# Optimization experiments

Measured on AMD Instinct MI355X. Metric: run time of the kernel, lower is better.

The kernel has to match this reference:

```python
import jax, jax.numpy as jnp
import numpy as np

SPATIAL_SHAPES = [(58, 100)]  # single level (H, W)
N_HEADS, N_LEVELS, N_POINTS, NUM_CAMS = 8, 1, 8, 6
D_MODEL = 256


def _bilinear_sample(v, loc, h, w):
    # v: (B, h, w, H, d); loc: (B, Lq, H, P, 2) normalized to [0,1]
    # matches F.grid_sample(mode='bilinear', padding_mode='zeros', align_corners=False)
    x = loc[..., 0] * w - 0.5
    y = loc[..., 1] * h - 0.5
    x0 = jnp.floor(x)
    y0 = jnp.floor(y)
    fx = x - x0
    fy = y - y0
    x0i = x0.astype(jnp.int32)
    y0i = y0.astype(jnp.int32)
    B, Hh = v.shape[0], v.shape[3]
    b = jnp.arange(B)[:, None, None, None]
    hd = jnp.arange(Hh)[None, None, :, None]

    def g(yi, xi):
        valid = ((yi >= 0) & (yi < h) & (xi >= 0) & (xi < w)).astype(v.dtype)
        yc = jnp.clip(yi, 0, h - 1)
        xc = jnp.clip(xi, 0, w - 1)
        return v[b, yc, xc, hd] * valid[..., None]  # (B,Lq,H,P,d)

    return (g(y0i, x0i) * ((1 - fy) * (1 - fx))[..., None]
            + g(y0i, x0i + 1) * ((1 - fy) * fx)[..., None]
            + g(y0i + 1, x0i) * (fy * (1 - fx))[..., None]
            + g(y0i + 1, x0i + 1) * (fy * fx)[..., None])


def _ms_deform_attn(value, locs, weights):
    # value: (B, S, H, d); locs: (B,Lq,H,L,P,2); weights: (B,Lq,H,L,P)
    B, S, Hh, d = value.shape
    out = 0.0
    start = 0
    for l, (h, w) in enumerate(SPATIAL_SHAPES):
        v = value[:, start:start + h * w].reshape(B, h, w, Hh, d)
        start += h * w
        samp = _bilinear_sample(v, locs[:, :, :, l], h, w)  # (B,Lq,H,P,d)
        out = out + jnp.einsum('bqhpd,bqhp->bqhd', samp, weights[:, :, :, l])
    return out.reshape(B, -1, Hh * d)


def setup_inputs() -> dict:
    key = jax.random.key(0)
    ks = jax.random.split(key, 12)
    B, Lq, C = 1, 22500, D_MODEL
    S = sum(h * w for h, w in SPATIAL_SHAPES)
    inp = {
        'query': jax.random.normal(ks[0], (B, Lq, C), jnp.float32),
        'reference_points_cam': jax.random.uniform(ks[1], (NUM_CAMS, B, Lq, 4, 2), jnp.float32),
        'bev_mask': jax.random.randint(ks[2], (NUM_CAMS, B, Lq, 4), 0, 2, jnp.int32),
        'value': jax.random.normal(ks[3], (B * NUM_CAMS, S, C), jnp.float32),
        'W_off': jax.random.normal(ks[4], (N_HEADS * N_LEVELS * N_POINTS * 2, C), jnp.float32) * 0.01,
        'b_off': jax.random.normal(ks[5], (N_HEADS * N_LEVELS * N_POINTS * 2,), jnp.float32),
        'W_attn': jax.random.normal(ks[6], (N_HEADS * N_LEVELS * N_POINTS, C), jnp.float32) * 0.02,
        'b_attn': jnp.zeros((N_HEADS * N_LEVELS * N_POINTS,), jnp.float32),
        'W_val': jax.random.normal(ks[7], (C, C), jnp.float32) * (1.0 / np.sqrt(C)),
        'b_val': jnp.zeros((C,), jnp.float32),
        'W_out': jax.random.normal(ks[8], (C, C), jnp.float32) * (1.0 / np.sqrt(C)),
        'b_out': jnp.zeros((C,), jnp.float32),
    }
    return inp


def reference(query, reference_points_cam, bev_mask, value,
              W_off, b_off, W_attn, b_attn, W_val, b_val, W_out, b_out):
    B, Lq, C = query.shape
    d = C // N_HEADS
    D = reference_points_cam.shape[3]  # num_Z_anchors = 4
    S = value.shape[1]

    # value_proj for all cameras; value rows are laid out as b*num_cams + cam
    val = value @ W_val.T + b_val
    val = val.reshape(B, NUM_CAMS, S, N_HEADS, d).transpose(1, 0, 2, 3, 4)  # (cams,B,S,H,d)

    # query-side projections are camera-independent
    off = (query @ W_off.T + b_off).reshape(B, Lq, N_HEADS, N_LEVELS, N_POINTS, 2)
    normalizer = jnp.array([[w, h] for (h, w) in SPATIAL_SHAPES], dtype=query.dtype)  # (L,2)
    off = off / normalizer[None, None, None, :, None, :]
    off = off.reshape(B, Lq, N_HEADS, N_LEVELS, N_POINTS // D, D, 2)

    aw = (query @ W_attn.T + b_attn).reshape(B, Lq, N_HEADS, N_LEVELS * N_POINTS)
    aw = jax.nn.softmax(aw, axis=-1).reshape(B, Lq, N_HEADS, N_LEVELS, N_POINTS)

    vis = (bev_mask.sum(-1) > 0)  # (cams, B, Lq)
    slots = jnp.zeros_like(query)
    for cam in range(NUM_CAMS):  # small fixed camera set
        ref = reference_points_cam[cam][:, :, None, None, None, :, :]  # (B,Lq,1,1,1,D,2)
        locs = (ref + off).reshape(B, Lq, N_HEADS, N_LEVELS, N_POINTS, 2)
        out = _ms_deform_attn(val[cam], locs, aw)  # (B,Lq,C)
        slots = slots + out * vis[cam][..., None].astype(query.dtype)

    count = jnp.maximum(vis.sum(0).astype(query.dtype), 1.0)  # (B,Lq)
    slots = slots / count[..., None]
    return slots @ W_out.T + b_out
```

## Files before the change

kernel.cpp:

```cpp
#include <hip/hip_runtime.h>

#define LQ     22500
#define SPA_H  58
#define SPA_W  100
#define S_TOT  5800
#define NCAMS  6
#define CDIM   256

typedef __attribute__((ext_vector_type(8))) _Float16 half8;
typedef __attribute__((ext_vector_type(4))) float f32x4;

__device__ __forceinline__ half8 cvt_f32x8(const float* p) {
  f32x4 a = *(const f32x4*)p;
  f32x4 b = *(const f32x4*)(p + 4);
  half8 r;
  r[0] = (_Float16)a.x; r[1] = (_Float16)a.y; r[2] = (_Float16)a.z; r[3] = (_Float16)a.w;
  r[4] = (_Float16)b.x; r[5] = (_Float16)b.y; r[6] = (_Float16)b.z; r[7] = (_Float16)b.w;
  return r;
}

__global__ __launch_bounds__(256) void cvt_weights_all(
    const float* __restrict__ Wv, const float* __restrict__ Wo,
    const float* __restrict__ Wf, const float* __restrict__ Wa,
    const float* __restrict__ bf, const float* __restrict__ ba,
    _Float16* __restrict__ dst, float* __restrict__ biascat) {
  const int i = blockIdx.x * 256 + threadIdx.x;
  if (i < 192) biascat[i] = (i < 128) ? bf[i] : ba[i - 128];
  if (i >= 180224) return;
  float v;
  if (i < 65536)       v = Wv[i];
  else if (i < 131072) v = Wo[i - 65536];
  else { const int j = i - 131072; v = (j < 32768) ? Wf[j] : Wa[j - 32768]; }
  dst[i] = (_Float16)v;
}

template<int N, bool A_F16, int OUT_MODE>
__global__ __launch_bounds__(256, 2) void gemm64(
    const void* __restrict__ Av, const _Float16* __restrict__ W,
    const float* __restrict__ bias, void* __restrict__ Cv, int M) {
  constexpr int K  = CDIM;
  constexpr int NT = (N / 4) / 16;
  const int lane = threadIdx.x & 63;
  const int wave = threadIdx.x >> 6;
  const int m15  = lane & 15;
  const int quad = lane >> 4;
  const int rowbase = blockIdx.x * 64;
  const int colbase = wave * (N / 4);

  f32x4 acc[4][NT];
#pragma unroll
  for (int rt = 0; rt < 4; ++rt)
#pragma unroll
    for (int t = 0; t < NT; ++t) acc[rt][t] = (f32x4){0.f, 0.f, 0.f, 0.f};

#pragma unroll
  for (int kk = 0; kk < K; kk += 32) {
    const int ko = kk + quad * 8;
    half8 a[4], b[NT];
#pragma unroll
    for (int rt = 0; rt < 4; ++rt) {
      int row = rowbase + rt * 16 + m15;
      row = row < M ? row : M - 1;
      if (A_F16) a[rt] = *(const half8*)((const _Float16*)Av + (size_t)row * K + ko);
      else       a[rt] = cvt_f32x8((const float*)Av + (size_t)row * K + ko);
    }
#pragma unroll
    for (int t = 0; t < NT; ++t)
      b[t] = *(const half8*)(W + (size_t)(colbase + t * 16 + m15) * K + ko);
#pragma unroll
    for (int t = 0; t < NT; ++t)
#pragma unroll
      for (int rt = 0; rt < 4; ++rt)
        acc[rt][t] = __builtin_amdgcn_mfma_f32_16x16x32_f16(a[rt], b[t], acc[rt][t], 0, 0, 0);
  }

#pragma unroll
  for (int rt = 0; rt < 4; ++rt) {
    const int orow = rowbase + rt * 16 + quad * 4;
#pragma unroll
    for (int t = 0; t < NT; ++t) {
      const int col = colbase + t * 16 + m15;
      const float bv = bias[col];
#pragma unroll
      for (int i = 0; i < 4; ++i) {
        const int r = orow + i;
        if (r < M) {
          const float v = acc[rt][t][i] + bv;
          if (OUT_MODE == 0) ((float*)Cv)[(size_t)r * N + col] = v;
          else               ((_Float16*)Cv)[(size_t)r * N + col] = (_Float16)v;
        }
      }
    }
  }
}

__global__ __launch_bounds__(128) void sampler(
    const _Float16* __restrict__ vp,
    const _Float16* __restrict__ qproj,
    const float* __restrict__ ref,
    const int* __restrict__ bev,
    _Float16* __restrict__ slots)
{
  const int t  = threadIdx.x;
  const int ql = t >> 4;
  const int s  = t & 15;
  const int h  = s >> 1;
  const int hf = s & 1;
  const int q  = blockIdx.x * 8 + ql;
  const bool qok = q < LQ;

  __shared__ float s_off[8][128];
  __shared__ float s_aw[8][64];
  __shared__ float s_ref[8][48];
  __shared__ int   s_vis[8][6];

  if (s < 6) s_vis[ql][s] = 0;
  if (qok) {
    const _Float16* qp = qproj + (size_t)q * 192;
#pragma unroll
    for (int rep = 0; rep < 12; ++rep) {
      const int j = s + rep * 16;
      const float v = (float)qp[j];
      if (j < 128) s_off[ql][j] = v * ((j & 1) ? (1.f / 58.f) : (1.f / 100.f));
      else         s_aw[ql][j - 128] = v;
    }
#pragma unroll
    for (int rep = 0; rep < 3; ++rep) {
      const int k = s + rep * 16;
      s_ref[ql][k] = ref[((size_t)(k >> 3) * LQ + q) * 8 + (k & 7)];
    }
    if (s < 6) {
      const int* bm = bev + ((size_t)s * LQ + q) * 4;
      s_vis[ql][s] = (bm[0] + bm[1] + bm[2] + bm[3]) > 0 ? 1 : 0;
    }
  }
  __syncthreads();

  float w8[8];
  {
    float m = -1e30f;
#pragma unroll
    for (int p = 0; p < 8; ++p) m = fmaxf(m, s_aw[ql][h * 8 + p]);
    float ssum = 0.f;
#pragma unroll
    for (int p = 0; p < 8; ++p) { w8[p] = __expf(s_aw[ql][h * 8 + p] - m); ssum += w8[p]; }
    const float inv = 1.f / ssum;
#pragma unroll
    for (int p = 0; p < 8; ++p) w8[p] *= inv;
  }

  int cnt = 0;
#pragma unroll
  for (int c = 0; c < 6; ++c) cnt += s_vis[ql][c];
  const float invc = 1.f / (float)(cnt > 0 ? cnt : 1);

  float acc[16];
#pragma unroll
  for (int i = 0; i < 16; ++i) acc[i] = 0.f;

  const int chbase = h * 32 + hf * 16;

#pragma unroll
  for (int cam = 0; cam < NCAMS; ++cam) {
    if (!s_vis[ql][cam]) continue;
    const _Float16* vpc = vp + (size_t)cam * (S_TOT * CDIM) + chbase;
#pragma unroll
    for (int p = 0; p < 8; ++p) {
      const int z = p & 3;
      const float lx = s_ref[ql][cam * 8 + z * 2 + 0] + s_off[ql][(h * 8 + p) * 2 + 0];
      const float ly = s_ref[ql][cam * 8 + z * 2 + 1] + s_off[ql][(h * 8 + p) * 2 + 1];
      const float x = lx * 100.f - 0.5f;
      const float y = ly * 58.f - 0.5f;
      const float x0f = floorf(x), y0f = floorf(y);
      const float fx = x - x0f, fy = y - y0f;
      const int x0 = (int)x0f, y0 = (int)y0f;
      const float wgt = w8[p];
      const float w00 = (1.f - fy) * (1.f - fx) * wgt;
      const float w01 = (1.f - fy) * fx * wgt;
      const float w10 = fy * (1.f - fx) * wgt;
      const float w11 = fy * fx * wgt;
      const bool xv0 = (x0 >= 0) && (x0 < SPA_W);
      const bool xv1 = (x0 + 1 >= 0) && (x0 + 1 < SPA_W);
#pragma unroll
      for (int dy = 0; dy < 2; ++dy) {
        const int yy = y0 + dy;
        if (yy < 0 || yy >= SPA_H) continue;
        const _Float16* rowp = vpc + (size_t)(yy * SPA_W) * CDIM;
        const float wl = dy ? w10 : w00;
        const float wr = dy ? w11 : w01;
        if (xv0) {
          const _Float16* tp = rowp + (size_t)x0 * CDIM;
          half8 v0 = *(const half8*)tp;
          half8 v1 = *(const half8*)(tp + 8);
#pragma unroll
          for (int i = 0; i < 8; ++i) acc[i]     = fmaf(wl, (float)v0[i], acc[i]);
#pragma unroll
          for (int i = 0; i < 8; ++i) acc[8 + i] = fmaf(wl, (float)v1[i], acc[8 + i]);
        }
        if (xv1) {
          const _Float16* tp = rowp + (size_t)(x0 + 1) * CDIM;
          half8 v0 = *(const half8*)tp;
          half8 v1 = *(const half8*)(tp + 8);
#pragma unroll
          for (int i = 0; i < 8; ++i) acc[i]     = fmaf(wr, (float)v0[i], acc[i]);
#pragma unroll
          for (int i = 0; i < 8; ++i) acc[8 + i] = fmaf(wr, (float)v1[i], acc[8 + i]);
        }
      }
    }
  }

  if (qok) {
    half8 o0, o1;
#pragma unroll
    for (int i = 0; i < 8; ++i) { o0[i] = (_Float16)(acc[i] * invc); o1[i] = (_Float16)(acc[8 + i] * invc); }
    _Float16* sp = slots + (size_t)q * CDIM + chbase;
    *(half8*)sp = o0;
    *(half8*)(sp + 8) = o1;
  }
}

extern "C" void kernel_launch(void* const* d_in, const int* in_sizes, int n_in,
                              void* d_out, int out_size, void* d_ws, size_t ws_size,
                              hipStream_t stream) {
  const float* query  = (const float*)d_in[0];
  const float* refpts = (const float*)d_in[1];
  const int*   bev    = (const int*)d_in[2];
  const float* value  = (const float*)d_in[3];
  const float* W_off  = (const float*)d_in[4];
  const float* b_off  = (const float*)d_in[5];
  const float* W_attn = (const float*)d_in[6];
  const float* b_attn = (const float*)d_in[7];
  const float* W_val  = (const float*)d_in[8];
  const float* b_val  = (const float*)d_in[9];
  const float* W_out  = (const float*)d_in[10];
  const float* b_out  = (const float*)d_in[11];

  char* ws = (char*)d_ws;
  _Float16* Wv_h    = (_Float16*)(ws + 0);
  _Float16* Wo_h    = (_Float16*)(ws + 131072);
  _Float16* Wcat_h  = (_Float16*)(ws + 262144);
  float*    biascat = (float*)   (ws + 360448);
  _Float16* vp      = (_Float16*)(ws + 361216);
  _Float16* qproj   = (_Float16*)(ws + 18178816);
  _Float16* slots   = (_Float16*)(ws + 26818816);

  cvt_weights_all<<<704, 256, 0, stream>>>(W_val, W_out, W_off, W_attn,
                                           b_off, b_attn, Wv_h, biascat);

  gemm64<256, false, 2><<<(34800 + 63) / 64, 256, 0, stream>>>(value, Wv_h, b_val, vp, 34800);
  gemm64<192, false, 2><<<(LQ + 63) / 64, 256, 0, stream>>>(query, Wcat_h, biascat, qproj, LQ);

  sampler<<<(LQ + 7) / 8, 128, 0, stream>>>(vp, qproj, refpts, bev, slots);

  gemm64<256, true, 0><<<(LQ + 63) / 64, 256, 0, stream>>>(slots, Wo_h, b_out, d_out, LQ);
}
```

Measured before the change: 370.9 us.

## Pre-convert inputs to fp16, fuse input GEMMs, pipeline K loop, branchless sampler

Converts value and query to fp16 in one vectorized pass, then runs the value and query projections in a single fused launch that writes results in place over the fp16 inputs, using a block barrier before the stores. The GEMM K loop is double-buffered with explicit load/MFMA interleaving. The sampler precomputes the softmax once per head in shared memory, uses clamped branchless bilinear taps with four loads issued together, and reuses the query buffer for slots. This reduces launches, workspace and f32 read traffic in the GEMMs and improves memory-level parallelism in the sampler, at the cost of an extra full conversion pass and aliasing risks.

```diff
diff --git a/kernel.cpp b/kernel.cpp
--- a/kernel.cpp
+++ b/kernel.cpp
@@ -8,44 +8,55 @@
 #define CDIM   256
 
 typedef __attribute__((ext_vector_type(8))) _Float16 half8;
+typedef __attribute__((ext_vector_type(4))) _Float16 half4;
 typedef __attribute__((ext_vector_type(4))) float f32x4;
 
-__device__ __forceinline__ half8 cvt_f32x8(const float* p) {
-  f32x4 a = *(const f32x4*)p;
-  f32x4 b = *(const f32x4*)(p + 4);
-  half8 r;
-  r[0] = (_Float16)a.x; r[1] = (_Float16)a.y; r[2] = (_Float16)a.z; r[3] = (_Float16)a.w;
-  r[4] = (_Float16)b.x; r[5] = (_Float16)b.y; r[6] = (_Float16)b.z; r[7] = (_Float16)b.w;
-  return r;
-}
-
-__global__ __launch_bounds__(256) void cvt_weights_all(
-    const float* __restrict__ Wv, const float* __restrict__ Wo,
-    const float* __restrict__ Wf, const float* __restrict__ Wa,
-    const float* __restrict__ bf, const float* __restrict__ ba,
-    _Float16* __restrict__ dst, float* __restrict__ biascat) {
-  const int i = blockIdx.x * 256 + threadIdx.x;
-  if (i < 192) biascat[i] = (i < 128) ? bf[i] : ba[i - 128];
-  if (i >= 180224) return;
-  float v;
-  if (i < 65536)       v = Wv[i];
-  else if (i < 131072) v = Wo[i - 65536];
-  else { const int j = i - 131072; v = (j < 32768) ? Wf[j] : Wa[j - 32768]; }
-  dst[i] = (_Float16)v;
-}
-
-template<int N, bool A_F16, int OUT_MODE>
-__global__ __launch_bounds__(256, 2) void gemm64(
-    const void* __restrict__ Av, const _Float16* __restrict__ W,
-    const float* __restrict__ bias, void* __restrict__ Cv, int M) {
-  constexpr int K  = CDIM;
-  constexpr int NT = (N / 4) / 16;
+__global__ __launch_bounds__(256) void cvt_all(
+    const float* __restrict__ value, const float* __restrict__ query,
+    const float* __restrict__ W_val, const float* __restrict__ W_off,
+    const float* __restrict__ W_attn, const float* __restrict__ W_out,
+    _Float16* __restrict__ val16, _Float16* __restrict__ q16,
+    _Float16* __restrict__ Wv, _Float16* __restrict__ Wcat,
+    _Float16* __restrict__ Wo) {
+  const long long e = ((long long)blockIdx.x * 256 + threadIdx.x) * 4;
+  const float* src; _Float16* dst; long long off;
+  if (e < 8908800)        { src = value;  dst = val16;        off = e; }
+  else if (e < 14668800)  { src = query;  dst = q16;          off = e - 8908800; }
+  else if (e < 14734336)  { src = W_val;  dst = Wv;           off = e - 14668800; }
+  else if (e < 14767104)  { src = W_off;  dst = Wcat;         off = e - 14734336; }
+  else if (e < 14783488)  { src = W_attn; dst = Wcat + 32768; off = e - 14767104; }
+  else if (e < 14849024)  { src = W_out;  dst = Wo;           off = e - 14783488; }
+  else return;
+  f32x4 v = *(const f32x4*)(src + off);
+  half4 o;
+  o[0] = (_Float16)v.x; o[1] = (_Float16)v.y; o[2] = (_Float16)v.z; o[3] = (_Float16)v.w;
+  *(half4*)(dst + off) = o;
+}
+
+template<int N, int OUT_MODE, bool INPLACE>
+__device__ __forceinline__ void gemm_body(
+    const _Float16* __restrict__ A, const _Float16* __restrict__ W,
+    const float* __restrict__ bias, const float* __restrict__ bias2,
+    void* __restrict__ Cv, int M, int rowbase) {
+  constexpr int NT = N / 64;
   const int lane = threadIdx.x & 63;
   const int wave = threadIdx.x >> 6;
   const int m15  = lane & 15;
   const int quad = lane >> 4;
-  const int rowbase = blockIdx.x * 64;
   const int colbase = wave * (N / 4);
+  const int kq = quad * 8;
+
+  const _Float16* ap[4];
+#pragma unroll
+  for (int rt = 0; rt < 4; ++rt) {
+    int r = rowbase + rt * 16 + m15;
+    r = r < M ? r : M - 1;
+    ap[rt] = A + (size_t)r * 256 + kq;
+  }
+  const _Float16* wp[NT];
+#pragma unroll
+  for (int t = 0; t < NT; ++t)
+    wp[t] = W + (size_t)(colbase + t * 16 + m15) * 256 + kq;
 
   f32x4 acc[4][NT];
 #pragma unroll
@@ -53,26 +64,30 @@
 #pragma unroll
     for (int t = 0; t < NT; ++t) acc[rt][t] = (f32x4){0.f, 0.f, 0.f, 0.f};
 
-#pragma unroll
-  for (int kk = 0; kk < K; kk += 32) {
-    const int ko = kk + quad * 8;
-    half8 a[4], b[NT];
-#pragma unroll
-    for (int rt = 0; rt < 4; ++rt) {
-      int row = rowbase + rt * 16 + m15;
-      row = row < M ? row : M - 1;
-      if (A_F16) a[rt] = *(const half8*)((const _Float16*)Av + (size_t)row * K + ko);
-      else       a[rt] = cvt_f32x8((const float*)Av + (size_t)row * K + ko);
-    }
-#pragma unroll
-    for (int t = 0; t < NT; ++t)
-      b[t] = *(const half8*)(W + (size_t)(colbase + t * 16 + m15) * K + ko);
-#pragma unroll
-    for (int t = 0; t < NT; ++t)
-#pragma unroll
-      for (int rt = 0; rt < 4; ++rt)
-        acc[rt][t] = __builtin_amdgcn_mfma_f32_16x16x32_f16(a[rt], b[t], acc[rt][t], 0, 0, 0);
-  }
+  half8 a0[4], b0[NT], a1[4], b1[NT];
+#define LOADSET(aa, bb, KO) \
+  { _Pragma("unroll") for (int rt = 0; rt < 4; ++rt) aa[rt] = *(const half8*)(ap[rt] + (KO)); \
+    _Pragma("unroll") for (int t = 0; t < NT; ++t)  bb[t]  = *(const half8*)(wp[t] + (KO)); }
+#define MFMASET(aa, bb) \
+  { _Pragma("unroll") for (int t = 0; t < NT; ++t) \
+      _Pragma("unroll") for (int rt = 0; rt < 4; ++rt) \
+        acc[rt][t] = __builtin_amdgcn_mfma_f32_16x16x32_f16(aa[rt], bb[t], acc[rt][t], 0, 0, 0); }
+
+  LOADSET(a0, b0, 0)
+#pragma unroll 1
+  for (int kk = 0; kk < 192; kk += 64) {
+    LOADSET(a1, b1, kk + 32)
+    MFMASET(a0, b0)
+    LOADSET(a0, b0, kk + 64)
+    MFMASET(a1, b1)
+  }
+  LOADSET(a1, b1, 224)
+  MFMASET(a0, b0)
+  MFMASET(a1, b1)
+#undef LOADSET
+#undef MFMASET
+
+  if (INPLACE) __syncthreads();
 
 #pragma unroll
   for (int rt = 0; rt < 4; ++rt) {
@@ -80,18 +95,35 @@
 #pragma unroll
     for (int t = 0; t < NT; ++t) {
       const int col = colbase + t * 16 + m15;
-      const float bv = bias[col];
+      const float bv = (N == 192 && col >= 128) ? bias2[col - 128] : bias[col];
 #pragma unroll
       for (int i = 0; i < 4; ++i) {
         const int r = orow + i;
         if (r < M) {
           const float v = acc[rt][t][i] + bv;
-          if (OUT_MODE == 0) ((float*)Cv)[(size_t)r * N + col] = v;
-          else               ((_Float16*)Cv)[(size_t)r * N + col] = (_Float16)v;
+          if (OUT_MODE == 0) ((float*)Cv)[(size_t)r * 256 + col] = v;
+          else               ((_Float16*)Cv)[(size_t)r * 256 + col] = (_Float16)v;
         }
       }
     }
   }
+}
+
+__global__ __launch_bounds__(256) void gemm_inputs(
+    const _Float16* __restrict__ val16, const _Float16* __restrict__ q16,
+    const _Float16* __restrict__ Wv, const _Float16* __restrict__ Wcat,
+    const float* __restrict__ b_val, const float* __restrict__ b_off,
+    const float* __restrict__ b_attn,
+    _Float16* __restrict__ vp, _Float16* __restrict__ qproj) {
+  const int b = blockIdx.x;
+  if (b < 544) gemm_body<256, 2, true>(val16, Wv, b_val, b_val, vp, 34800, b * 64);
+  else         gemm_body<192, 2, true>(q16, Wcat, b_off, b_attn, qproj, LQ, (b - 544) * 64);
+}
+
+__global__ __launch_bounds__(256) void gemm_out_k(
+    const _Float16* __restrict__ slots, const _Float16* __restrict__ Wo,
+    const float* __restrict__ b_out, float* __restrict__ out) {
+  gemm_body<256, 0, false>(slots, Wo, b_out, b_out, out, LQ, blockIdx.x * 64);
 }
 
 __global__ __launch_bounds__(128) void sampler(
@@ -105,49 +137,49 @@
   const int ql = t >> 4;
   const int s  = t & 15;
   const int h  = s >> 1;
-  const int hf = s & 1;
   const int q  = blockIdx.x * 8 + ql;
   const bool qok = q < LQ;
 
-  __shared__ float s_off[8][128];
-  __shared__ float s_aw[8][64];
+  __shared__ float s_off[8][8][17];
+  __shared__ float s_w8[8][8][9];
   __shared__ float s_ref[8][48];
   __shared__ int   s_vis[8][6];
 
-  if (s < 6) s_vis[ql][s] = 0;
   if (qok) {
-    const _Float16* qp = qproj + (size_t)q * 192;
-#pragma unroll
-    for (int rep = 0; rep < 12; ++rep) {
-      const int j = s + rep * 16;
-      const float v = (float)qp[j];
-      if (j < 128) s_off[ql][j] = v * ((j & 1) ? (1.f / 58.f) : (1.f / 100.f));
-      else         s_aw[ql][j - 128] = v;
-    }
-#pragma unroll
-    for (int rep = 0; rep < 3; ++rep) {
-      const int k = s + rep * 16;
-      s_ref[ql][k] = ref[((size_t)(k >> 3) * LQ + q) * 8 + (k & 7)];
+    const _Float16* qp = qproj + (size_t)q * 256;
+    {
+      half8 oc = *(const half8*)(qp + s * 8);
+#pragma unroll
+      for (int i = 0; i < 8; ++i) {
+        const int f = s * 8 + i;
+        s_off[ql][f >> 4][f & 15] =
+            (float)oc[i] * ((f & 1) ? (1.f / 58.f) : (1.f / 100.f));
+      }
+    }
+    if (s < 8) {
+      half8 aw = *(const half8*)(qp + 128 + s * 8);
+      float m = -1e30f;
+#pragma unroll
+      for (int p = 0; p < 8; ++p) m = fmaxf(m, (float)aw[p]);
+      float e[8], ssum = 0.f;
+#pragma unroll
+      for (int p = 0; p < 8; ++p) { e[p] = __expf((float)aw[p] - m); ssum += e[p]; }
+      const float inv = 1.f / ssum;
+#pragma unroll
+      for (int p = 0; p < 8; ++p) s_w8[ql][s][p] = e[p] * inv;
+    }
+    if (s < 12) {
+      const int cam = s >> 1, hf = s & 1;
+      f32x4 r = *(const f32x4*)(ref + ((size_t)cam * LQ + q) * 8 + hf * 4);
+      *(f32x4*)&s_ref[ql][s * 4] = r;
     }
     if (s < 6) {
-      const int* bm = bev + ((size_t)s * LQ + q) * 4;
-      s_vis[ql][s] = (bm[0] + bm[1] + bm[2] + bm[3]) > 0 ? 1 : 0;
+      int4 bm = *(const int4*)(bev + ((size_t)s * LQ + q) * 4);
+      s_vis[ql][s] = (bm.x + bm.y + bm.z + bm.w) > 0 ? 1 : 0;
     }
   }
   __syncthreads();
-
-  float w8[8];
-  {
-    float m = -1e30f;
-#pragma unroll
-    for (int p = 0; p < 8; ++p) m = fmaxf(m, s_aw[ql][h * 8 + p]);
-    float ssum = 0.f;
-#pragma unroll
-    for (int p = 0; p < 8; ++p) { w8[p] = __expf(s_aw[ql][h * 8 + p] - m); ssum += w8[p]; }
-    const float inv = 1.f / ssum;
-#pragma unroll
-    for (int p = 0; p < 8; ++p) w8[p] *= inv;
-  }
+  if (!qok) return;
 
   int cnt = 0;
 #pragma unroll
@@ -158,66 +190,68 @@
 #pragma unroll
   for (int i = 0; i < 16; ++i) acc[i] = 0.f;
 
-  const int chbase = h * 32 + hf * 16;
-
-#pragma unroll
+#pragma unroll 1
   for (int cam = 0; cam < NCAMS; ++cam) {
     if (!s_vis[ql][cam]) continue;
-    const _Float16* vpc = vp + (size_t)cam * (S_TOT * CDIM) + chbase;
-#pragma unroll
-    for (int p = 0; p < 8; ++p) {
-      const int z = p & 3;
-      const float lx = s_ref[ql][cam * 8 + z * 2 + 0] + s_off[ql][(h * 8 + p) * 2 + 0];
-      const float ly = s_ref[ql][cam * 8 + z * 2 + 1] + s_off[ql][(h * 8 + p) * 2 + 1];
-      const float x = lx * 100.f - 0.5f;
-      const float y = ly * 58.f - 0.5f;
-      const float x0f = floorf(x), y0f = floorf(y);
-      const float fx = x - x0f, fy = y - y0f;
-      const int x0 = (int)x0f, y0 = (int)y0f;
-      const float wgt = w8[p];
-      const float w00 = (1.f - fy) * (1.f - fx) * wgt;
-      const float w01 = (1.f - fy) * fx * wgt;
-      const float w10 = fy * (1.f - fx) * wgt;
-      const float w11 = fy * fx * wgt;
-      const bool xv0 = (x0 >= 0) && (x0 < SPA_W);
-      const bool xv1 = (x0 + 1 >= 0) && (x0 + 1 < SPA_W);
-#pragma unroll
-      for (int dy = 0; dy < 2; ++dy) {
-        const int yy = y0 + dy;
-        if (yy < 0 || yy >= SPA_H) continue;
-        const _Float16* rowp = vpc + (size_t)(yy * SPA_W) * CDIM;
-        const float wl = dy ? w10 : w00;
-        const float wr = dy ? w11 : w01;
-        if (xv0) {
-          const _Float16* tp = rowp + (size_t)x0 * CDIM;
-          half8 v0 = *(const half8*)tp;
-          half8 v1 = *(const half8*)(tp + 8);
-#pragma unroll
-          for (int i = 0; i < 8; ++i) acc[i]     = fmaf(wl, (float)v0[i], acc[i]);
-#pragma unroll
-          for (int i = 0; i < 8; ++i) acc[8 + i] = fmaf(wl, (float)v1[i], acc[8 + i]);
+    const _Float16* vpc = vp + (size_t)cam * (S_TOT * CDIM) + s * 16;
+
+#pragma unroll 1
+    for (int pp = 0; pp < 4; ++pp) {
+      half8 v[16];
+      float w[8];
+#pragma unroll
+      for (int j = 0; j < 2; ++j) {
+        const int p = pp * 2 + j;
+        const int z = p & 3;
+        const float x = (s_ref[ql][cam * 8 + z * 2 + 0] + s_off[ql][h][p * 2 + 0]) * 100.f - 0.5f;
+        const float y = (s_ref[ql][cam * 8 + z * 2 + 1] + s_off[ql][h][p * 2 + 1]) * 58.f - 0.5f;
+        const float x0f = floorf(x), y0f = floorf(y);
+        const float fx = x - x0f, fy = y - y0f;
+        const int x0 = (int)x0f, y0 = (int)y0f;
+        const float vx0 = (x0 >= 0 && x0 < SPA_W) ? 1.f : 0.f;
+        const float vx1 = (x0 >= -1 && x0 < SPA_W - 1) ? 1.f : 0.f;
+        const float vy0 = (y0 >= 0 && y0 < SPA_H) ? 1.f : 0.f;
+        const float vy1 = (y0 >= -1 && y0 < SPA_H - 1) ? 1.f : 0.f;
+        const int xc0 = min(max(x0, 0), SPA_W - 1), xc1 = min(max(x0 + 1, 0), SPA_W - 1);
+        const int yc0 = min(max(y0, 0), SPA_H - 1), yc1 = min(max(y0 + 1, 0), SPA_H - 1);
+        const float wgt = s_w8[ql][h][p];
+        const float wy0 = (1.f - fy) * wgt, wy1 = fy * wgt;
+        w[j * 4 + 0] = wy0 * (1.f - fx) * vy0 * vx0;
+        w[j * 4 + 1] = wy0 * fx * vy0 * vx1;
+        w[j * 4 + 2] = wy1 * (1.f - fx) * vy1 * vx0;
+        w[j * 4 + 3] = wy1 * fx * vy1 * vx1;
+        const _Float16* t00 = vpc + (size_t)(yc0 * SPA_W + xc0) * CDIM;
+        const _Float16* t01 = vpc + (size_t)(yc0 * SPA_W + xc1) * CDIM;
+        const _Float16* t10 = vpc + (size_t)(yc1 * SPA_W + xc0) * CDIM;
+        const _Float16* t11 = vpc + (size_t)(yc1 * SPA_W + xc1) * CDIM;
+        v[j * 8 + 0] = *(const half8*)t00; v[j * 8 + 1] = *(const half8*)(t00 + 8);
+        v[j * 8 + 2] = *(const half8*)t01; v[j * 8 + 3] = *(const half8*)(t01 + 8);
+        v[j * 8 + 4] = *(const half8*)t10; v[j * 8 + 5] = *(const half8*)(t10 + 8);
+        v[j * 8 + 6] = *(const half8*)t11; v[j * 8 + 7] = *(const half8*)(t11 + 8);
+      }
+#pragma unroll
+      for (int j = 0; j < 2; ++j)
+#pragma unroll
+        for (int tap = 0; tap < 4; ++tap) {
+          const float wk = w[j * 4 + tap];
+#pragma unroll
+          for (int i = 0; i < 8; ++i) {
+            acc[i]     = fmaf(wk, (float)v[j * 8 + tap * 2][i],     acc[i]);
+            acc[8 + i] = fmaf(wk, (float)v[j * 8 + tap * 2 + 1][i], acc[8 + i]);
+          }
         }
-        if (xv1) {
-          const _Float16* tp = rowp + (size_t)(x0 + 1) * CDIM;
-          half8 v0 = *(const half8*)tp;
-          half8 v1 = *(const half8*)(tp + 8);
-#pragma unroll
-          for (int i = 0; i < 8; ++i) acc[i]     = fmaf(wr, (float)v0[i], acc[i]);
-#pragma unroll
-          for (int i = 0; i < 8; ++i) acc[8 + i] = fmaf(wr, (float)v1[i], acc[8 + i]);
-        }
-      }
-    }
-  }
-
-  if (qok) {
-    half8 o0, o1;
-#pragma unroll
-    for (int i = 0; i < 8; ++i) { o0[i] = (_Float16)(acc[i] * invc); o1[i] = (_Float16)(acc[8 + i] * invc); }
-    _Float16* sp = slots + (size_t)q * CDIM + chbase;
-    *(half8*)sp = o0;
-    *(half8*)(sp + 8) = o1;
-  }
+    }
+  }
+
+  half8 o0, o1;
+#pragma unroll
+  for (int i = 0; i < 8; ++i) {
+    o0[i] = (_Float16)(acc[i] * invc);
+    o1[i] = (_Float16)(acc[8 + i] * invc);
+  }
+  _Float16* sp = slots + (size_t)q * 256 + s * 16;
+  *(half8*)sp = o0;
+  *(half8*)(sp + 8) = o1;
 }
 
 extern "C" void kernel_launch(void* const* d_in, const int* in_sizes, int n_in,
@@ -237,21 +271,19 @@
   const float* b_out  = (const float*)d_in[11];
 
   char* ws = (char*)d_ws;
-  _Float16* Wv_h    = (_Float16*)(ws + 0);
-  _Float16* Wo_h    = (_Float16*)(ws + 131072);
-  _Float16* Wcat_h  = (_Float16*)(ws + 262144);
-  float*    biascat = (float*)   (ws + 360448);
-  _Float16* vp      = (_Float16*)(ws + 361216);
-  _Float16* qproj   = (_Float16*)(ws + 18178816);
-  _Float16* slots   = (_Float16*)(ws + 26818816);
-
-  cvt_weights_all<<<704, 256, 0, stream>>>(W_val, W_out, W_off, W_attn,
-                                           b_off, b_attn, Wv_h, biascat);
-
-  gemm64<256, false, 2><<<(34800 + 63) / 64, 256, 0, stream>>>(value, Wv_h, b_val, vp, 34800);
-  gemm64<192, false, 2><<<(LQ + 63) / 64, 256, 0, stream>>>(query, Wcat_h, biascat, qproj, LQ);
-
-  sampler<<<(LQ + 7) / 8, 128, 0, stream>>>(vp, qproj, refpts, bev, slots);
-
-  gemm64<256, true, 0><<<(LQ + 63) / 64, 256, 0, stream>>>(slots, Wo_h, b_out, d_out, LQ);
-}
+  _Float16* val16 = (_Float16*)(ws + 0);
+  _Float16* q16   = (_Float16*)(ws + 17817600);
+  _Float16* Wv    = (_Float16*)(ws + 29337600);
+  _Float16* Wcat  = (_Float16*)(ws + 29468672);
+  _Float16* Wo    = (_Float16*)(ws + 29566976);
+
+  cvt_all<<<14501, 256, 0, stream>>>(value, query, W_val, W_off, W_attn, W_out,
+                                     val16, q16, Wv, Wcat, Wo);
+
+  gemm_inputs<<<896, 256, 0, stream>>>(val16, q16, Wv, Wcat,
+                                       b_val, b_off, b_attn, val16, q16);
+
+  sampler<<<(LQ + 7) / 8, 128, 0, stream>>>(val16, q16, refpts, bev, q16);
+
+  gemm_out_k<<<(LQ + 63) / 64, 256, 0, stream>>>(q16, Wo, b_out, (float*)d_out);
+}
```

Result: slower. 408.4 us (+10.1%).
